# Kernel tuning notes

Measured on AMD Instinct MI355X. Metric: run time of the kernel, lower is better.

Reference implementation:

```python
import jax, jax.numpy as jnp
import numpy as np

BATCH = 4096
DIM = 128
TEMPERATURE = 0.1


def setup_inputs() -> dict:
    key = jax.random.key(0)
    k1, k2 = jax.random.split(key)
    out1 = jax.random.normal(k1, (BATCH, DIM), dtype=jnp.float32)
    out2 = jax.random.normal(k2, (BATCH, DIM), dtype=jnp.float32)
    return {"out1": out1, "out2": out2}


def reference(out1, out2):
    B = out1.shape[0]
    total = jnp.concatenate([out1, out2], axis=0)                 # [2B, D]
    total = total / jnp.linalg.norm(total, axis=1, keepdims=True)  # L2 normalize rows
    sim = jnp.matmul(total, total.T) / TEMPERATURE                 # [2B, 2B]
    # mask the diagonal with -1e9 (matches masked_fill_ with float('-1e9'))
    diag_mask = jnp.eye(2 * B, dtype=bool)
    sim = jnp.where(diag_mask, jnp.float32(-1e9), sim)
    log_prob = -jax.nn.log_softmax(sim, axis=1)                    # [2B, 2B]
    # vectorized positive-pair diagonal gather: (k, B+k) and (B+k, k)
    idx = jnp.arange(B)
    pos = log_prob[idx, idx + B] + log_prob[idx + B, idx]          # [B]
    loss = jnp.sum(pos)
    # faithful to original: loss / 2 * batch_size == (loss / 2) * B
    return loss / 2 * B
```

## Files before the change

kernel.cpp:

```cpp
#include <hip/hip_runtime.h>
#include <hip/hip_bf16.h>
#include <cstdint>


typedef __bf16 bf16x8 __attribute__((ext_vector_type(8)));
typedef __bf16 bf16x2 __attribute__((ext_vector_type(2)));
typedef float  f32x4  __attribute__((ext_vector_type(4)));

#define NROWS 8192
#define DIM   128
#define ALPHA 3.7982827f
#define LN2   0.6931471805599453f

__device__ __forceinline__ void load_lds16(const void* g, void* l) {
    __builtin_amdgcn_global_load_lds(
        (const __attribute__((address_space(1))) unsigned int*)(uintptr_t)g,
        (__attribute__((address_space(3))) unsigned int*)(uintptr_t)l,
        16, 0, 0);
}


__global__ __launch_bounds__(256) void norm_kernel(
    const float* __restrict__ out1, const float* __restrict__ out2,
    __bf16* __restrict__ nb, float* __restrict__ rowsum, float* __restrict__ dout)
{
    const int t = threadIdx.x, lane = t & 63, wid = t >> 6;
    const int row = blockIdx.x * 4 + wid;
    const float* src = (row < 4096) ? (out1 + (size_t)row * DIM)
                                    : (out2 + (size_t)(row - 4096) * DIM);
    float2 v = ((const float2*)src)[lane];
    float ss = v.x * v.x + v.y * v.y;
    #pragma unroll
    for (int off = 1; off < 64; off <<= 1) ss += __shfl_xor(ss, off);
    const float s = rsqrtf(ss) * ALPHA;

    const int c  = lane >> 2;
    const int cs = (c & 8) | ((c ^ row) & 7);
    const int idx = row * DIM + cs * 8 + ((2 * lane) & 7);
    bf16x2 w;
    w.x = (__bf16)(v.x * s);
    w.y = (__bf16)(v.y * s);
    *(bf16x2*)(nb + idx) = w;

    if (blockIdx.x < 32) rowsum[blockIdx.x * 256 + t] = 0.0f;
    if (blockIdx.x == 0 && t == 0) dout[0] = 0.0f;
}

__global__ __launch_bounds__(256, 2) void simloss_main(
    const __bf16* __restrict__ nb, float* __restrict__ rowsum)
{
    __shared__ __bf16 Bsm[128 * DIM];
    const int t = threadIdx.x, lane = t & 63, wid = t >> 6;
    const int quad = lane >> 4, l15 = lane & 15;
    const int rb = blockIdx.x, cb = blockIdx.y;
    const int rowbase = rb * 128 + (wid & 1) * 64;
    const int ncol0   = (wid >> 1) * 64;

    int cso[4];
    #pragma unroll
    for (int k = 0; k < 4; ++k) {
        int c = k * 4 + quad;
        cso[k] = ((c & 8) | ((c ^ lane) & 7)) * 8;
    }

    bf16x8 afrag[4][4];
    #pragma unroll
    for (int mt = 0; mt < 4; ++mt) {
        const __bf16* ar = nb + (size_t)(rowbase + mt * 16 + l15) * DIM;
        #pragma unroll
        for (int k = 0; k < 4; ++k) afrag[mt][k] = *(const bf16x8*)(ar + cso[k]);
    }

    float rowpart[4][4] = {};

    for (int ct = 0; ct < 8; ++ct) {
        __syncthreads();
        const char* gB = (const char*)(nb + (size_t)(cb * 1024 + ct * 128) * DIM);
        char* lB = (char*)Bsm + wid * 1024;
        const char* gBw = gB + wid * 1024 + lane * 16;
        #pragma unroll
        for (int i = 0; i < 8; ++i) load_lds16(gBw + i * 4096, lB + i * 4096);
        __syncthreads();

        f32x4 acc[4][4] = {};
        #pragma unroll
        for (int k = 0; k < 4; ++k) {
            bf16x8 b[4];
            #pragma unroll
            for (int nt = 0; nt < 4; ++nt)
                b[nt] = *(const bf16x8*)(Bsm + (ncol0 + nt * 16 + l15) * DIM + cso[k]);
            #pragma unroll
            for (int mt = 0; mt < 4; ++mt)
                #pragma unroll
                for (int nt = 0; nt < 4; ++nt)
                    acc[mt][nt] = __builtin_amdgcn_mfma_f32_16x16x32_bf16(
                        afrag[mt][k], b[nt], acc[mt][nt], 0, 0, 0);
        }

        #pragma unroll
        for (int mt = 0; mt < 4; ++mt)
            #pragma unroll
            for (int nt = 0; nt < 4; ++nt)
                #pragma unroll
                for (int r = 0; r < 4; ++r)
                    rowpart[mt][r] += __builtin_amdgcn_exp2f(acc[mt][nt][r]);
    }

    #pragma unroll
    for (int mt = 0; mt < 4; ++mt)
        #pragma unroll
        for (int r = 0; r < 4; ++r) {
            float v = rowpart[mt][r];
            v += __shfl_xor(v, 1);
            v += __shfl_xor(v, 2);
            v += __shfl_xor(v, 4);
            v += __shfl_xor(v, 8);
            if (l15 == 0)
                atomicAdd(&rowsum[rowbase + mt * 16 + quad * 4 + r], v);
        }
}

__global__ __launch_bounds__(256) void finalize_kernel(
    const __bf16* __restrict__ nb, const float* __restrict__ rowsum,
    float* __restrict__ dout)
{
    const int t = threadIdx.x, lane = t & 63, wid = t >> 6;
    const int w = blockIdx.x * 4 + wid;
    float wacc = 0.0f;
    for (int rr = 0; rr < 16; ++rr) {
        const int i = w * 16 + rr;
        const int p = i ^ 4096;
        bf16x2 av = *(const bf16x2*)(nb + (size_t)i * DIM + 2 * lane);
        bf16x2 bv = *(const bf16x2*)(nb + (size_t)p * DIM + 2 * lane);
        float ax = (float)av.x, ay = (float)av.y;
        float bx = (float)bv.x, by = (float)bv.y;
        float self = ax * ax + ay * ay;
        float pos  = ax * bx + ay * by;
        #pragma unroll
        for (int off = 1; off < 64; off <<= 1) {
            self += __shfl_xor(self, off);
            pos  += __shfl_xor(pos, off);
        }
        if (lane == 0) {
            float se = rowsum[i] - __builtin_amdgcn_exp2f(self);
            wacc += logf(se) - pos * LN2;
        }
    }
    if (lane == 0) atomicAdd(dout, wacc * 2048.0f);
}

extern "C" void kernel_launch(void* const* d_in, const int* in_sizes, int n_in,
                              void* d_out, int out_size, void* d_ws, size_t ws_size,
                              hipStream_t stream)
{
    const float* out1 = (const float*)d_in[0];
    const float* out2 = (const float*)d_in[1];
    __bf16* nb     = (__bf16*)d_ws;
    float*  rowsum = (float*)((char*)d_ws + (size_t)NROWS * DIM * 2);
    float*  dout   = (float*)d_out;

    hipLaunchKernelGGL(norm_kernel, dim3(2048), dim3(256), 0, stream,
                       out1, out2, nb, rowsum, dout);
    hipLaunchKernelGGL(simloss_main, dim3(64, 8), dim3(256), 0, stream,
                       (const __bf16*)nb, rowsum);
    hipLaunchKernelGGL(finalize_kernel, dim3(128), dim3(256), 0, stream,
                       (const __bf16*)nb, rowsum, dout);
}
```

Before: 91.29 us.

## Stage A tile in LDS and replace rowsum atomics with per-slot partial writes

The A row tile now goes into LDS through global_load_lds, and each k-step reads fragments from there, so the block no longer keeps 16 bf16x8 A fragments in registers. The launch-bounds occupancy hint is dropped and LDS per block doubles. Row partial sums go to 16 separate slots per row instead of float atomics, which also removes the rowsum zeroing in norm_kernel. Finalize reduces the 16 slots with shuffles and uses twice as many blocks. The trade is extra LDS reads per k-step and lower possible occupancy, in exchange for fewer registers and no atomic contention.

```diff
diff --git a/kernel.cpp b/kernel.cpp
--- a/kernel.cpp
+++ b/kernel.cpp
@@ -22,7 +22,7 @@
 
 __global__ __launch_bounds__(256) void norm_kernel(
     const float* __restrict__ out1, const float* __restrict__ out2,
-    __bf16* __restrict__ nb, float* __restrict__ rowsum, float* __restrict__ dout)
+    __bf16* __restrict__ nb, float* __restrict__ dout)
 {
     const int t = threadIdx.x, lane = t & 63, wid = t >> 6;
     const int row = blockIdx.x * 4 + wid;
@@ -42,19 +42,19 @@
     w.y = (__bf16)(v.y * s);
     *(bf16x2*)(nb + idx) = w;
 
-    if (blockIdx.x < 32) rowsum[blockIdx.x * 256 + t] = 0.0f;
     if (blockIdx.x == 0 && t == 0) dout[0] = 0.0f;
 }
 
-__global__ __launch_bounds__(256, 2) void simloss_main(
+__global__ __launch_bounds__(256) void simloss_main(
     const __bf16* __restrict__ nb, float* __restrict__ rowsum)
 {
+    __shared__ __bf16 Asm[128 * DIM];
     __shared__ __bf16 Bsm[128 * DIM];
     const int t = threadIdx.x, lane = t & 63, wid = t >> 6;
     const int quad = lane >> 4, l15 = lane & 15;
     const int rb = blockIdx.x, cb = blockIdx.y;
-    const int rowbase = rb * 128 + (wid & 1) * 64;
-    const int ncol0   = (wid >> 1) * 64;
+    const int rloc  = (wid & 1) * 64;
+    const int ncol0 = (wid >> 1) * 64;
 
     int cso[4];
     #pragma unroll
@@ -63,29 +63,31 @@
         cso[k] = ((c & 8) | ((c ^ lane) & 7)) * 8;
     }
 
-    bf16x8 afrag[4][4];
-    #pragma unroll
-    for (int mt = 0; mt < 4; ++mt) {
-        const __bf16* ar = nb + (size_t)(rowbase + mt * 16 + l15) * DIM;
+    {
+        const char* gA = (const char*)(nb + (size_t)rb * 128 * DIM) + wid * 1024 + lane * 16;
+        char* lA = (char*)Asm + wid * 1024;
         #pragma unroll
-        for (int k = 0; k < 4; ++k) afrag[mt][k] = *(const bf16x8*)(ar + cso[k]);
+        for (int i = 0; i < 8; ++i) load_lds16(gA + i * 4096, lA + i * 4096);
     }
 
     float rowpart[4][4] = {};
 
     for (int ct = 0; ct < 8; ++ct) {
         __syncthreads();
-        const char* gB = (const char*)(nb + (size_t)(cb * 1024 + ct * 128) * DIM);
+        const char* gB = (const char*)(nb + (size_t)(cb * 1024 + ct * 128) * DIM)
+                         + wid * 1024 + lane * 16;
         char* lB = (char*)Bsm + wid * 1024;
-        const char* gBw = gB + wid * 1024 + lane * 16;
         #pragma unroll
-        for (int i = 0; i < 8; ++i) load_lds16(gBw + i * 4096, lB + i * 4096);
+        for (int i = 0; i < 8; ++i) load_lds16(gB + i * 4096, lB + i * 4096);
         __syncthreads();
 
         f32x4 acc[4][4] = {};
         #pragma unroll
         for (int k = 0; k < 4; ++k) {
-            bf16x8 b[4];
+            bf16x8 a[4], b[4];
+            #pragma unroll
+            for (int mt = 0; mt < 4; ++mt)
+                a[mt] = *(const bf16x8*)(Asm + (rloc + mt * 16 + l15) * DIM + cso[k]);
             #pragma unroll
             for (int nt = 0; nt < 4; ++nt)
                 b[nt] = *(const bf16x8*)(Bsm + (ncol0 + nt * 16 + l15) * DIM + cso[k]);
@@ -94,7 +96,7 @@
                 #pragma unroll
                 for (int nt = 0; nt < 4; ++nt)
                     acc[mt][nt] = __builtin_amdgcn_mfma_f32_16x16x32_bf16(
-                        afrag[mt][k], b[nt], acc[mt][nt], 0, 0, 0);
+                        a[mt], b[nt], acc[mt][nt], 0, 0, 0);
         }
 
         #pragma unroll
@@ -106,6 +108,7 @@
                     rowpart[mt][r] += __builtin_amdgcn_exp2f(acc[mt][nt][r]);
     }
 
+    const int slot = cb * 2 + (wid >> 1);
     #pragma unroll
     for (int mt = 0; mt < 4; ++mt)
         #pragma unroll
@@ -115,8 +118,10 @@
             v += __shfl_xor(v, 2);
             v += __shfl_xor(v, 4);
             v += __shfl_xor(v, 8);
-            if (l15 == 0)
-                atomicAdd(&rowsum[rowbase + mt * 16 + quad * 4 + r], v);
+            if (l15 == 0) {
+                int grow = rb * 128 + rloc + mt * 16 + quad * 4 + r;
+                rowsum[grow * 16 + slot] = v;
+            }
         }
 }
 
@@ -127,8 +132,8 @@
     const int t = threadIdx.x, lane = t & 63, wid = t >> 6;
     const int w = blockIdx.x * 4 + wid;
     float wacc = 0.0f;
-    for (int rr = 0; rr < 16; ++rr) {
-        const int i = w * 16 + rr;
+    for (int rr = 0; rr < 8; ++rr) {
+        const int i = w * 8 + rr;
         const int p = i ^ 4096;
         bf16x2 av = *(const bf16x2*)(nb + (size_t)i * DIM + 2 * lane);
         bf16x2 bv = *(const bf16x2*)(nb + (size_t)p * DIM + 2 * lane);
@@ -136,15 +141,15 @@
         float bx = (float)bv.x, by = (float)bv.y;
         float self = ax * ax + ay * ay;
         float pos  = ax * bx + ay * by;
+        float se   = (lane < 16) ? rowsum[(size_t)i * 16 + lane] : 0.0f;
         #pragma unroll
         for (int off = 1; off < 64; off <<= 1) {
             self += __shfl_xor(self, off);
             pos  += __shfl_xor(pos, off);
+            se   += __shfl_xor(se, off);
         }
-        if (lane == 0) {
-            float se = rowsum[i] - __builtin_amdgcn_exp2f(self);
-            wacc += logf(se) - pos * LN2;
-        }
+        if (lane == 0)
+            wacc += logf(se - __builtin_amdgcn_exp2f(self)) - pos * LN2;
     }
     if (lane == 0) atomicAdd(dout, wacc * 2048.0f);
 }
@@ -160,9 +165,9 @@
     float*  dout   = (float*)d_out;
 
     hipLaunchKernelGGL(norm_kernel, dim3(2048), dim3(256), 0, stream,
-                       out1, out2, nb, rowsum, dout);
+                       out1, out2, nb, dout);
     hipLaunchKernelGGL(simloss_main, dim3(64, 8), dim3(256), 0, stream,
                        (const __bf16*)nb, rowsum);
-    hipLaunchKernelGGL(finalize_kernel, dim3(128), dim3(256), 0, stream,
+    hipLaunchKernelGGL(finalize_kernel, dim3(256), dim3(256), 0, stream,
                        (const __bf16*)nb, rowsum, dout);
 }
```

After: 97.54 us. +6.8%, slower.
